# Performance work log

Hardware: AMD Instinct MI355X
Metric: run time of the kernel (lower is better)

Reference implementation:

```python
import jax, jax.numpy as jnp
import numpy as np

C = 16          # cardinality (hard-coded in GraphHead)
E = 1024        # node_encoding_size == representation_size (residual requires equality)
S = 1024        # spatial_head output size (hard-coded Linear(256,1024))
R = 1024        # representation_size
D = R // C      # sub_repr_size = 64
NS, NO = 64, 256
NUM_ITER = 2
EPS = 1e-5


def _w(key, shape, fan_in):
    return jax.random.normal(key, shape, dtype=jnp.float32) * np.float32((2.0 / fan_in) ** 0.5)


def setup_inputs() -> dict:
    key = jax.random.key(0)
    ks = jax.random.split(key, 16)
    inp = {
        'h': jax.random.normal(ks[0], (NS, E), dtype=jnp.float32),
        'o': jax.random.normal(ks[1], (NO, E), dtype=jnp.float32),
        'spatial': jax.random.normal(ks[2], (NS, NO, S), dtype=jnp.float32),
        # attention_head: MultiBranchFusion(2E, 1024, R, 16)
        'att_w1': _w(ks[3], (C, 2 * E, D), 2 * E), 'att_b1': jnp.zeros((C, D), jnp.float32),
        'att_w2': _w(ks[4], (C, S, D), S),         'att_b2': jnp.zeros((C, D), jnp.float32),
        'att_w3': _w(ks[5], (C, D, R), D),         'att_b3': jnp.zeros((C, R), jnp.float32),
        # sub_to_obj: MessageMBF(E, 1024, R, 'subject', 16)
        's2o_w1': _w(ks[6], (C, E, D), E),         's2o_b1': jnp.zeros((C, D), jnp.float32),
        's2o_w2': _w(ks[7], (C, S, D), S),         's2o_b2': jnp.zeros((C, D), jnp.float32),
        's2o_w3': _w(ks[8], (C, D, R), D),         's2o_b3': jnp.zeros((C, R), jnp.float32),
        # obj_to_sub: MessageMBF(E, 1024, R, 'object', 16)
        'o2s_w1': _w(ks[9], (C, E, D), E),         'o2s_b1': jnp.zeros((C, D), jnp.float32),
        'o2s_w2': _w(ks[10], (C, S, D), S),        'o2s_b2': jnp.zeros((C, D), jnp.float32),
        'o2s_w3': _w(ks[11], (C, D, R), D),        'o2s_b3': jnp.zeros((C, R), jnp.float32),
        # adjacency: Linear(R, 1)
        'adj_w': _w(ks[12], (R, 1), R), 'adj_b': jnp.zeros((1,), jnp.float32),
        # LayerNorms
        'ns_g': jnp.ones((E,), jnp.float32), 'ns_b': jnp.zeros((E,), jnp.float32),
        'no_g': jnp.ones((E,), jnp.float32), 'no_b': jnp.zeros((E,), jnp.float32),
    }
    return inp


def _layernorm(x, g, b):
    m = jnp.mean(x, axis=-1, keepdims=True)
    v = jnp.mean((x - m) ** 2, axis=-1, keepdims=True)
    return (x - m) * jax.lax.rsqrt(v + EPS) * g + b


def _mbf_pair(app, spa, w1, b1, w2, b2, w3, b3):
    # app [ns,no,A], spa [ns,no,S] -> [ns,no,R]; sum over C branches of fc3(relu(fc1*fc2))
    a = jnp.einsum('ija,cad->cijd', app, w1) + b1[:, None, None, :]
    s = jnp.einsum('ijs,csd->cijd', spa, w2) + b2[:, None, None, :]
    g = jax.nn.relu(a * s)
    return jnp.einsum('cijd,cdr->ijr', g, w3) + b3.sum(0)


def _msg_subject(h, spa, w1, b1, w2, b2, w3, b3):
    # MessageMBF subject: broadcast fc1(h) [ns,d] against fc2(spa) [ns,no,d]
    a = jnp.einsum('ia,cad->cid', h, w1) + b1[:, None, :]
    s = jnp.einsum('ijs,csd->cijd', spa, w2) + b2[:, None, None, :]
    g = jax.nn.relu(a[:, :, None, :] * s)
    return jnp.einsum('cijd,cdr->ijr', g, w3) + b3.sum(0)  # [ns,no,R]


def _msg_object(o, spa, w1, b1, w2, b2, w3, b3):
    # MessageMBF object: broadcast fc1(o) [no,d] against fc2(spa) [ns,no,d]
    a = jnp.einsum('ja,cad->cjd', o, w1) + b1[:, None, :]
    s = jnp.einsum('ijs,csd->cijd', spa, w2) + b2[:, None, None, :]
    g = jax.nn.relu(a[:, None, :, :] * s)
    return jnp.einsum('cijd,cdr->ijr', g, w3) + b3.sum(0)  # [ns,no,R]


def reference(h, o, spatial,
              att_w1, att_b1, att_w2, att_b2, att_w3, att_b3,
              s2o_w1, s2o_b1, s2o_w2, s2o_b2, s2o_w3, s2o_b3,
              o2s_w1, o2s_b1, o2s_w2, o2s_b2, o2s_w3, o2s_b3,
              adj_w, adj_b, ns_g, ns_b, no_g, no_b):
    ns, no = h.shape[0], o.shape[0]
    for _ in range(NUM_ITER):
        # edge weights via attention MBF on concatenated pair encodings
        pair_app = jnp.concatenate([
            jnp.broadcast_to(h[:, None, :], (ns, no, E)),
            jnp.broadcast_to(o[None, :, :], (ns, no, E)),
        ], axis=-1)
        w = jax.nn.relu(_mbf_pair(pair_app, spatial, att_w1, att_b1, att_w2, att_b2, att_w3, att_b3))
        adj = jnp.einsum('ijr,rk->ij', w, adj_w) + adj_b[0]  # [ns,no]
        # update subject nodes from object messages
        m_o2s = _msg_object(o, spatial, o2s_w1, o2s_b1, o2s_w2, o2s_b2, o2s_w3, o2s_b3)
        msg_h = jax.nn.relu(jnp.einsum('ij,ijr->ir', jax.nn.softmax(adj, axis=1), m_o2s))
        h = _layernorm(h + msg_h, ns_g, ns_b)
        # update object nodes from (updated) subject messages
        m_s2o = _msg_subject(h, spatial, s2o_w1, s2o_b1, s2o_w2, s2o_b2, s2o_w3, s2o_b3)
        msg_o = jax.nn.relu(jnp.einsum('ij,ijr->jr', jax.nn.softmax(adj, axis=0), m_s2o))
        o = _layernorm(o + msg_o, no_g, no_b)
    return jnp.concatenate([h, o], axis=0)  # [ns+no, E]
```

## Files before the change

kernel.cpp:

```cpp
#include <hip/hip_runtime.h>
#include <cstdint>
#include <cstddef>

typedef _Float16 hf;
typedef _Float16 h8v __attribute__((ext_vector_type(8)));
typedef float f4v __attribute__((ext_vector_type(4)));

#define NS 64
#define NO 256
#define MP 16384
#define KD 1024

__device__ __forceinline__ h8v cvt8(float4 a, float4 b) {
    h8v r;
    r[0] = (hf)a.x; r[1] = (hf)a.y; r[2] = (hf)a.z; r[3] = (hf)a.w;
    r[4] = (hf)b.x; r[5] = (hf)b.y; r[6] = (hf)b.z; r[7] = (hf)b.w;
    return r;
}
__device__ __forceinline__ float f4at(const float4& a, const float4& b, int e) {
    const float* p = e < 4 ? (const float*)&a : (const float*)&b;
    return p[e & 3];
}

__global__ void k_reorder16(const float* __restrict__ src, hf* __restrict__ dhi,
                            hf* __restrict__ dlo, int Asrc, int aOff) {
    __shared__ float tile[64][65];
    int c = blockIdx.x, a0 = blockIdx.y * 64;
    int t = threadIdx.x, lx = t & 63, ly = t >> 6;
#pragma unroll
    for (int p = 0; p < 16; ++p) {
        int ar = ly + p * 4;
        tile[ar][lx] = src[(size_t)(c * Asrc + aOff + a0 + ar) * 64 + lx];
    }
    __syncthreads();
#pragma unroll
    for (int p = 0; p < 16; ++p) {
        int d = ly + p * 4;
        float v = tile[lx][d];
        hf h = (hf)v;
        size_t idx = (size_t)(c * 64 + d) * 1024 + a0 + lx;
        dhi[idx] = h;
        if (dlo) dlo[idx] = (hf)(v - (float)h);
    }
}

__global__ void k_transpose16(const float* __restrict__ src, hf* __restrict__ dhi,
                              hf* __restrict__ dlo) {
    __shared__ float tile[64][65];
    int r0 = blockIdx.x * 64, s0 = blockIdx.y * 64;
    int t = threadIdx.x, lx = t & 63, ly = t >> 6;
#pragma unroll
    for (int p = 0; p < 16; ++p) {
        int srow = ly + p * 4;
        tile[srow][lx] = src[(size_t)(s0 + srow) * 1024 + r0 + lx];
    }
    __syncthreads();
#pragma unroll
    for (int p = 0; p < 16; ++p) {
        int rr = ly + p * 4;
        float v = tile[lx][rr];
        hf h = (hf)v;
        size_t idx = (size_t)(r0 + rr) * 1024 + s0 + lx;
        dhi[idx] = h;
        if (dlo) dlo[idx] = (hf)(v - (float)h);
    }
}

__global__ void k_prep_bc(const float* __restrict__ ab2, const float* __restrict__ ob2,
                          const float* __restrict__ sb2, const float* __restrict__ ab3,
                          const float* __restrict__ ob3, const float* __restrict__ sb3,
                          float* __restrict__ b2cat, float* __restrict__ b3a,
                          float* __restrict__ b3o, float* __restrict__ b3s) {
    int g = blockIdx.x * 256 + threadIdx.x;
    if (g >= 1024) return;
    b2cat[g] = ab2[g]; b2cat[1024 + g] = ob2[g]; b2cat[2048 + g] = sb2[g];
    float sa = 0.f, so = 0.f, ss = 0.f;
    for (int c = 0; c < 16; ++c) {
        sa += ab3[c * 1024 + g];
        so += ob3[c * 1024 + g];
        ss += sb3[c * 1024 + g];
    }
    b3a[g] = sa; b3o[g] = so; b3s[g] = ss;
}

__global__ void k_init_ho(const float* __restrict__ h, const float* __restrict__ o,
                          float* __restrict__ outbuf, hf* __restrict__ h16, hf* __restrict__ o16) {
    int g = blockIdx.x * 256 + threadIdx.x;
    if (g < NS * KD) { float v = h[g]; outbuf[g] = v; h16[g] = (hf)v; }
    int g2 = g - NS * KD;
    if (g2 >= 0 && g2 < NO * KD) { float v = o[g2]; outbuf[NS * KD + g2] = v; o16[g2] = (hf)v; }
}

__global__ __launch_bounds__(256) void k_prep_gemm(
    const float* __restrict__ sp,
    const hf* __restrict__ Wah, const hf* __restrict__ Wal,
    const hf* __restrict__ Wo2, const hf* __restrict__ Ws2,
    const float* __restrict__ b2cat,
    hf* __restrict__ Sh, hf* __restrict__ Sl,
    hf* __restrict__ So, hf* __restrict__ Ss) {
    __shared__ hf Ah[4096];
    __shared__ hf Bh[4096];
    __shared__ hf Bl[4096];
    const int tid = threadIdx.x;
    int lin = blockIdx.y * 24 + blockIdx.x;
    int xcd = lin & 7, slot = lin >> 3;
    int xn = slot % 24;
    const int plane = xn >> 3;
    const int nloc = (xn & 7) * 128;
    const int m0 = ((xcd << 4) + slot / 24) * 128;
    const hf* Bb = plane == 0 ? Wah : (plane == 1 ? Wo2 : Ws2);
    const bool hasL = (plane == 0);
    const int lane = tid & 63, wid = tid >> 6;
    const int wm = wid >> 1, wn = wid & 1;
    const int lr = lane & 15, lg = lane >> 4;
    const int srow = tid >> 2, sseg = tid & 3;
    const int wo_ = srow * 32 + (sseg ^ ((srow >> 1) & 3)) * 8;
    const int rsl = (lg ^ ((lr >> 1) & 3)) * 8;

    f4v acc[4][4];
    f4v zz; zz[0] = 0.f; zz[1] = 0.f; zz[2] = 0.f; zz[3] = 0.f;
#pragma unroll
    for (int a = 0; a < 4; ++a)
#pragma unroll
        for (int b = 0; b < 4; ++b) acc[a][b] = zz;

    const float* pa0 = sp + (size_t)(m0 + srow) * KD + sseg * 8;
    const float* pa1 = sp + (size_t)(m0 + 64 + srow) * KD + sseg * 8;
    const hf* pb0 = Bb + (size_t)(nloc + srow) * KD + sseg * 8;
    const hf* pb1 = Bb + (size_t)(nloc + 64 + srow) * KD + sseg * 8;
    const hf* ql0 = Wal + (size_t)(nloc + srow) * KD + sseg * 8;
    const hf* ql1 = Wal + (size_t)(nloc + 64 + srow) * KD + sseg * 8;

    float4 a00, a01, a10, a11;
    h8v vb0, vb1, wb0, wb1;
    auto LOAD = [&](int kk) {
        a00 = *(const float4*)(pa0 + kk); a01 = *(const float4*)(pa0 + kk + 4);
        a10 = *(const float4*)(pa1 + kk); a11 = *(const float4*)(pa1 + kk + 4);
        vb0 = *(const h8v*)(pb0 + kk); vb1 = *(const h8v*)(pb1 + kk);
        if (hasL) { wb0 = *(const h8v*)(ql0 + kk); wb1 = *(const h8v*)(ql1 + kk); }
    };
    LOAD(0);
    for (int t = 0; t < 32; ++t) {
        __syncthreads();
        *(h8v*)(Ah + wo_) = cvt8(a00, a01);
        *(h8v*)(Ah + 2048 + wo_) = cvt8(a10, a11);
        *(h8v*)(Bh + wo_) = vb0; *(h8v*)(Bh + 2048 + wo_) = vb1;
        if (hasL) { *(h8v*)(Bl + wo_) = wb0; *(h8v*)(Bl + 2048 + wo_) = wb1; }
        __syncthreads();
        if (t + 1 < 32) LOAD((t + 1) * 32);
        h8v fa[4], fb[4];
#pragma unroll
        for (int x = 0; x < 4; ++x) {
            fa[x] = *(const h8v*)(Ah + (wm * 64 + x * 16 + lr) * 32 + rsl);
            fb[x] = *(const h8v*)(Bh + (wn * 64 + x * 16 + lr) * 32 + rsl);
        }
#pragma unroll
        for (int mi = 0; mi < 4; ++mi)
#pragma unroll
            for (int ni = 0; ni < 4; ++ni)
                acc[mi][ni] = __builtin_amdgcn_mfma_f32_16x16x32_f16(fa[mi], fb[ni], acc[mi][ni], 0, 0, 0);
        if (hasL) {
#pragma unroll
            for (int x = 0; x < 4; ++x)
                fb[x] = *(const h8v*)(Bl + (wn * 64 + x * 16 + lr) * 32 + rsl);
#pragma unroll
            for (int mi = 0; mi < 4; ++mi)
#pragma unroll
                for (int ni = 0; ni < 4; ++ni)
                    acc[mi][ni] = __builtin_amdgcn_mfma_f32_16x16x32_f16(fa[mi], fb[ni], acc[mi][ni], 0, 0, 0);
        }
    }
#pragma unroll
    for (int mi = 0; mi < 4; ++mi)
#pragma unroll
        for (int ni = 0; ni < 4; ++ni)
#pragma unroll
            for (int r = 0; r < 4; ++r) {
                int gr = m0 + wm * 64 + mi * 16 + lg * 4 + r;
                int col = nloc + wn * 64 + ni * 16 + lr;
                float v = acc[mi][ni][r] + b2cat[plane * 1024 + col];
                size_t idx = (size_t)gr * KD + col;
                if (plane == 0) {
                    hf hi = (hf)v;
                    Sh[idx] = hi; Sl[idx] = (hf)(v - (float)hi);
                } else if (plane == 1) So[idx] = (hf)v;
                else Ss[idx] = (hf)v;
            }
}

__global__ void k_build_g(const hf* __restrict__ Sh, const hf* __restrict__ Sl,
                          const float* __restrict__ e1, const float* __restrict__ e2,
                          hf* __restrict__ Gh, hf* __restrict__ Gl) {
    int g = blockIdx.x * 256 + threadIdx.x;
    size_t base = (size_t)g * 8;
    int m = (int)(base >> 10);
    int k = (int)(base & 1023);
    int i = m >> 8, j = m & 255;
    h8v sh = *(const h8v*)(Sh + base);
    h8v sl = *(const h8v*)(Sl + base);
    float4 ex0 = *(const float4*)(e1 + (size_t)i * KD + k);
    float4 ex1 = *(const float4*)(e1 + (size_t)i * KD + k + 4);
    float4 ey0 = *(const float4*)(e2 + (size_t)j * KD + k);
    float4 ey1 = *(const float4*)(e2 + (size_t)j * KD + k + 4);
    h8v gh, gl;
#pragma unroll
    for (int e = 0; e < 8; ++e) {
        float s = (float)sh[e] + (float)sl[e];
        float ee = f4at(ex0, ex1, e) + f4at(ey0, ey1, e);
        float gg = ee * s; gg = gg > 0.f ? gg : 0.f;
        hf hi = (hf)gg; gh[e] = hi; gl[e] = (hf)(gg - (float)hi);
    }
    *(h8v*)(Gh + base) = gh;
    *(h8v*)(Gl + base) = gl;
}

__global__ __launch_bounds__(256) void k_adj_gemm(
    const hf* __restrict__ Gh, const hf* __restrict__ Gl,
    const hf* __restrict__ W3h, const hf* __restrict__ W3l,
    const float* __restrict__ b3, const float* __restrict__ aw,
    float* __restrict__ adjv) {
    __shared__ hf Ah[4096];
    __shared__ hf Al[4096];
    __shared__ hf Bh[4096];
    __shared__ hf Bl[4096];
    const int tid = threadIdx.x;
    int lin = blockIdx.y * 8 + blockIdx.x;
    int xcd = lin & 7, slot = lin >> 3;
    const int n0 = (slot & 7) * 128;
    const int m0 = ((xcd << 4) + (slot >> 3)) * 128;
    const int lane = tid & 63, wid = tid >> 6;
    const int wm = wid >> 1, wn = wid & 1;
    const int lr = lane & 15, lg = lane >> 4;
    const int srow = tid >> 2, sseg = tid & 3;
    const int wo_ = srow * 32 + (sseg ^ ((srow >> 1) & 3)) * 8;
    const int rsl = (lg ^ ((lr >> 1) & 3)) * 8;
    const int ar0 = m0 + srow, ar1 = ar0 + 64;
    const int ko = sseg * 8;

    f4v acc[4][4];
    f4v zz; zz[0] = 0.f; zz[1] = 0.f; zz[2] = 0.f; zz[3] = 0.f;
#pragma unroll
    for (int a = 0; a < 4; ++a)
#pragma unroll
        for (int b = 0; b < 4; ++b) acc[a][b] = zz;

    h8v va0, va1, ua0, ua1, vb0, vb1, wb0, wb1;
    auto LOAD = [&](int kk) {
        va0 = *(const h8v*)(Gh + (size_t)ar0 * KD + ko + kk);
        va1 = *(const h8v*)(Gh + (size_t)ar1 * KD + ko + kk);
        ua0 = *(const h8v*)(Gl + (size_t)ar0 * KD + ko + kk);
        ua1 = *(const h8v*)(Gl + (size_t)ar1 * KD + ko + kk);
        vb0 = *(const h8v*)(W3h + (size_t)(n0 + srow) * KD + ko + kk);
        vb1 = *(const h8v*)(W3h + (size_t)(n0 + 64 + srow) * KD + ko + kk);
        wb0 = *(const h8v*)(W3l + (size_t)(n0 + srow) * KD + ko + kk);
        wb1 = *(const h8v*)(W3l + (size_t)(n0 + 64 + srow) * KD + ko + kk);
    };
    LOAD(0);
    for (int t = 0; t < 32; ++t) {
        __syncthreads();
        *(h8v*)(Ah + wo_) = va0; *(h8v*)(Ah + 2048 + wo_) = va1;
        *(h8v*)(Al + wo_) = ua0; *(h8v*)(Al + 2048 + wo_) = ua1;
        *(h8v*)(Bh + wo_) = vb0; *(h8v*)(Bh + 2048 + wo_) = vb1;
        *(h8v*)(Bl + wo_) = wb0; *(h8v*)(Bl + 2048 + wo_) = wb1;
        __syncthreads();
        if (t + 1 < 32) LOAD((t + 1) * 32);
        h8v fa[4], fb[4];
#pragma unroll
        for (int x = 0; x < 4; ++x) {
            fa[x] = *(const h8v*)(Ah + (wm * 64 + x * 16 + lr) * 32 + rsl);
            fb[x] = *(const h8v*)(Bh + (wn * 64 + x * 16 + lr) * 32 + rsl);
        }
#pragma unroll
        for (int mi = 0; mi < 4; ++mi)
#pragma unroll
            for (int ni = 0; ni < 4; ++ni)
                acc[mi][ni] = __builtin_amdgcn_mfma_f32_16x16x32_f16(fa[mi], fb[ni], acc[mi][ni], 0, 0, 0);
#pragma unroll
        for (int x = 0; x < 4; ++x)
            fb[x] = *(const h8v*)(Bl + (wn * 64 + x * 16 + lr) * 32 + rsl);
#pragma unroll
        for (int mi = 0; mi < 4; ++mi)
#pragma unroll
            for (int ni = 0; ni < 4; ++ni)
                acc[mi][ni] = __builtin_amdgcn_mfma_f32_16x16x32_f16(fa[mi], fb[ni], acc[mi][ni], 0, 0, 0);
#pragma unroll
        for (int x = 0; x < 4; ++x) {
            fa[x] = *(const h8v*)(Al + (wm * 64 + x * 16 + lr) * 32 + rsl);
            fb[x] = *(const h8v*)(Bh + (wn * 64 + x * 16 + lr) * 32 + rsl);
        }
#pragma unroll
        for (int mi = 0; mi < 4; ++mi)
#pragma unroll
            for (int ni = 0; ni < 4; ++ni)
                acc[mi][ni] = __builtin_amdgcn_mfma_f32_16x16x32_f16(fa[mi], fb[ni], acc[mi][ni], 0, 0, 0);
    }
    float b3v[4], awv[4];
#pragma unroll
    for (int ni = 0; ni < 4; ++ni) {
        int gc = n0 + wn * 64 + ni * 16 + lr;
        b3v[ni] = b3[gc]; awv[ni] = aw[gc];
    }
#pragma unroll
    for (int mi = 0; mi < 4; ++mi)
#pragma unroll
        for (int r = 0; r < 4; ++r) {
            float part = 0.f;
#pragma unroll
            for (int ni = 0; ni < 4; ++ni) {
                float w = acc[mi][ni][r] + b3v[ni];
                w = w > 0.f ? w : 0.f;
                part += w * awv[ni];
            }
            part += __shfl_xor(part, 1);
            part += __shfl_xor(part, 2);
            part += __shfl_xor(part, 4);
            part += __shfl_xor(part, 8);
            if (lr == 0) atomicAdd(adjv + m0 + wm * 64 + mi * 16 + lg * 4 + r, part);
        }
}

struct SRoute { const hf* A; const hf* Bh; const hf* Bl; float* C; const float* bias; int m0; int M; };
struct SRoutes { SRoute r[5]; };

__global__ __launch_bounds__(256) void k_small(SRoutes RR) {
    const SRoute rt = RR.r[blockIdx.y];
    __shared__ hf Ah[4096];
    __shared__ hf Bh[4096];
    __shared__ hf Bl[4096];
    const int tid = threadIdx.x;
    const int n0 = blockIdx.x * 128;
    const int kbeg = blockIdx.z * 128;
    const int lane = tid & 63, wid = tid >> 6;
    const int wm = wid >> 1, wn = wid & 1;
    const int lr = lane & 15, lg = lane >> 4;
    const int srow = tid >> 2, sseg = tid & 3;
    const int wo_ = srow * 32 + (sseg ^ ((srow >> 1) & 3)) * 8;
    const int rsl = (lg ^ ((lr >> 1) & 3)) * 8;
    int ar0 = rt.m0 + srow;      if (ar0 >= rt.M) ar0 = rt.M - 1;
    int ar1 = rt.m0 + 64 + srow; if (ar1 >= rt.M) ar1 = rt.M - 1;
    const bool hasL = rt.Bl != nullptr;
    const int ko = kbeg + sseg * 8;

    f4v acc[4][4];
    f4v zz; zz[0] = 0.f; zz[1] = 0.f; zz[2] = 0.f; zz[3] = 0.f;
#pragma unroll
    for (int a = 0; a < 4; ++a)
#pragma unroll
        for (int b = 0; b < 4; ++b) acc[a][b] = zz;

    h8v va0, va1, vb0, vb1, wb0, wb1;
    auto LOAD = [&](int kk) {
        va0 = *(const h8v*)(rt.A + (size_t)ar0 * KD + ko + kk);
        va1 = *(const h8v*)(rt.A + (size_t)ar1 * KD + ko + kk);
        vb0 = *(const h8v*)(rt.Bh + (size_t)(n0 + srow) * KD + ko + kk);
        vb1 = *(const h8v*)(rt.Bh + (size_t)(n0 + 64 + srow) * KD + ko + kk);
        if (hasL) {
            wb0 = *(const h8v*)(rt.Bl + (size_t)(n0 + srow) * KD + ko + kk);
            wb1 = *(const h8v*)(rt.Bl + (size_t)(n0 + 64 + srow) * KD + ko + kk);
        }
    };
    LOAD(0);
    for (int t = 0; t < 4; ++t) {
        __syncthreads();
        *(h8v*)(Ah + wo_) = va0; *(h8v*)(Ah + 2048 + wo_) = va1;
        *(h8v*)(Bh + wo_) = vb0; *(h8v*)(Bh + 2048 + wo_) = vb1;
        if (hasL) { *(h8v*)(Bl + wo_) = wb0; *(h8v*)(Bl + 2048 + wo_) = wb1; }
        __syncthreads();
        if (t + 1 < 4) LOAD((t + 1) * 32);
        h8v fa[4], fb[4];
#pragma unroll
        for (int x = 0; x < 4; ++x) {
            fa[x] = *(const h8v*)(Ah + (wm * 64 + x * 16 + lr) * 32 + rsl);
            fb[x] = *(const h8v*)(Bh + (wn * 64 + x * 16 + lr) * 32 + rsl);
        }
#pragma unroll
        for (int mi = 0; mi < 4; ++mi)
#pragma unroll
            for (int ni = 0; ni < 4; ++ni)
                acc[mi][ni] = __builtin_amdgcn_mfma_f32_16x16x32_f16(fa[mi], fb[ni], acc[mi][ni], 0, 0, 0);
        if (hasL) {
#pragma unroll
            for (int x = 0; x < 4; ++x)
                fb[x] = *(const h8v*)(Bl + (wn * 64 + x * 16 + lr) * 32 + rsl);
#pragma unroll
            for (int mi = 0; mi < 4; ++mi)
#pragma unroll
                for (int ni = 0; ni < 4; ++ni)
                    acc[mi][ni] = __builtin_amdgcn_mfma_f32_16x16x32_f16(fa[mi], fb[ni], acc[mi][ni], 0, 0, 0);
        }
    }
#pragma unroll
    for (int mi = 0; mi < 4; ++mi)
#pragma unroll
        for (int ni = 0; ni < 4; ++ni)
#pragma unroll
            for (int r = 0; r < 4; ++r) {
                int gr = rt.m0 + wm * 64 + mi * 16 + lg * 4 + r;
                int gc = n0 + wn * 64 + ni * 16 + lr;
                if (gr < rt.M) {
                    float v = acc[mi][ni][r];
                    if (rt.bias && blockIdx.z == 0) v += rt.bias[gc];
                    atomicAdd(rt.C + (size_t)gr * KD + gc, v);
                }
            }
}

__global__ void k_softmax_rows(const float* __restrict__ adj, float* __restrict__ p) {
    __shared__ float red[256];
    int i = blockIdx.x, j = threadIdx.x;
    float x = adj[i * 256 + j];
    red[j] = x; __syncthreads();
    for (int s = 128; s > 0; s >>= 1) { if (j < s) red[j] = fmaxf(red[j], red[j + s]); __syncthreads(); }
    float mx = red[0]; __syncthreads();
    float e = __expf(x - mx);
    red[j] = e; __syncthreads();
    for (int s = 128; s > 0; s >>= 1) { if (j < s) red[j] += red[j + s]; __syncthreads(); }
    p[i * 256 + j] = e / red[0];
}

__global__ void k_softmax_cols(const float* __restrict__ adj, float* __restrict__ q) {
    int j = blockIdx.x, i = threadIdx.x;
    float x = adj[i * 256 + j];
    float mx = x;
#pragma unroll
    for (int off = 32; off > 0; off >>= 1) mx = fmaxf(mx, __shfl_xor(mx, off));
    float e = __expf(x - mx);
    float s = e;
#pragma unroll
    for (int off = 32; off > 0; off >>= 1) s += __shfl_xor(s, off);
    q[i * 256 + j] = e / s;
}

__global__ void k_build_Gh(const hf* __restrict__ S, const float* __restrict__ aF,
                           const float* __restrict__ p, hf* __restrict__ Gh) {
    __shared__ float pl[256];
    int i = blockIdx.x;
    int k = blockIdx.y * 256 + threadIdx.x;
    pl[threadIdx.x] = p[i * 256 + threadIdx.x];
    __syncthreads();
    const hf* sp = S + (size_t)(i * 256) * KD + k;
    float acc = 0.f;
#pragma unroll 4
    for (int j = 0; j < 256; ++j) {
        float a = aF[(size_t)j * KD + k];
        float s = (float)sp[(size_t)j * KD];
        float g = a * s; g = g > 0.f ? g : 0.f;
        acc += pl[j] * g;
    }
    Gh[(size_t)i * KD + k] = (hf)acc;
}

__global__ void k_build_Go(const hf* __restrict__ S, const float* __restrict__ aF,
                           const float* __restrict__ q, hf* __restrict__ Go) {
    __shared__ float ql[64];
    int j = blockIdx.x;
    int k = blockIdx.y * 256 + threadIdx.x;
    if (threadIdx.x < 64) ql[threadIdx.x] = q[threadIdx.x * 256 + j];
    __syncthreads();
    const hf* sp = S + (size_t)j * KD + k;
    float acc = 0.f;
#pragma unroll 4
    for (int i = 0; i < 64; ++i) {
        float a = aF[(size_t)i * KD + k];
        float s = (float)sp[(size_t)(i * 256) * KD];
        float g = a * s; g = g > 0.f ? g : 0.f;
        acc += ql[i] * g;
    }
    Go[(size_t)j * KD + k] = (hf)acc;
}

__global__ void k_ln_update(float* __restrict__ x, const float* __restrict__ msg,
                            const float* __restrict__ b3, const float* __restrict__ gamma,
                            const float* __restrict__ beta, hf* __restrict__ x16) {
    __shared__ float red[256];
    int r = blockIdx.x, t = threadIdx.x;
    float v[4];
    float s = 0.f;
#pragma unroll
    for (int e = 0; e < 4; ++e) {
        int idx = t + e * 256;
        float mm = msg[(size_t)r * KD + idx] + b3[idx];
        mm = mm > 0.f ? mm : 0.f;
        v[e] = x[(size_t)r * KD + idx] + mm;
        s += v[e];
    }
    red[t] = s; __syncthreads();
    for (int st = 128; st > 0; st >>= 1) { if (t < st) red[t] += red[t + st]; __syncthreads(); }
    float mean = red[0] * (1.f / 1024.f);
    __syncthreads();
    float s2 = 0.f;
#pragma unroll
    for (int e = 0; e < 4; ++e) { float d = v[e] - mean; s2 += d * d; }
    red[t] = s2; __syncthreads();
    for (int st = 128; st > 0; st >>= 1) { if (t < st) red[t] += red[t + st]; __syncthreads(); }
    float var = red[0] * (1.f / 1024.f);
    float rstd = rsqrtf(var + 1e-5f);
#pragma unroll
    for (int e = 0; e < 4; ++e) {
        int idx = t + e * 256;
        float y = (v[e] - mean) * rstd * gamma[idx] + beta[idx];
        x[(size_t)r * KD + idx] = y;
        x16[(size_t)r * KD + idx] = (hf)y;
    }
}

extern "C" void kernel_launch(void* const* d_in, const int* in_sizes, int n_in,
                              void* d_out, int out_size, void* d_ws, size_t ws_size,
                              hipStream_t stream) {
    const float* h_in    = (const float*)d_in[0];
    const float* o_in    = (const float*)d_in[1];
    const float* spatial = (const float*)d_in[2];
    const float* att_w1  = (const float*)d_in[3];
    const float* att_b1  = (const float*)d_in[4];
    const float* att_w2  = (const float*)d_in[5];
    const float* att_b2  = (const float*)d_in[6];
    const float* att_w3  = (const float*)d_in[7];
    const float* att_b3  = (const float*)d_in[8];
    const float* s2o_w1  = (const float*)d_in[9];
    const float* s2o_b1  = (const float*)d_in[10];
    const float* s2o_w2  = (const float*)d_in[11];
    const float* s2o_b2  = (const float*)d_in[12];
    const float* s2o_w3  = (const float*)d_in[13];
    const float* s2o_b3  = (const float*)d_in[14];
    const float* o2s_w1  = (const float*)d_in[15];
    const float* o2s_b1  = (const float*)d_in[16];
    const float* o2s_w2  = (const float*)d_in[17];
    const float* o2s_b2  = (const float*)d_in[18];
    const float* o2s_w3  = (const float*)d_in[19];
    const float* o2s_b3  = (const float*)d_in[20];
    const float* adj_w   = (const float*)d_in[21];
    const float* ns_g    = (const float*)d_in[23];
    const float* ns_b    = (const float*)d_in[24];
    const float* no_g    = (const float*)d_in[25];
    const float* no_b    = (const float*)d_in[26];

    char* ws = (char*)d_ws;
    size_t off = 0;
    auto alloc = [&](size_t bytes) -> char* {
        char* pp = ws + off;
        off += (bytes + 255) & ~(size_t)255;
        return pp;
    };
    const size_t PLANE = (size_t)MP * KD * sizeof(hf);
    const size_t WMAT  = (size_t)1024 * 1024 * sizeof(hf);
    hf* S_att_h = (hf*)alloc(PLANE);
    hf* S_att_l = (hf*)alloc(PLANE);
    hf* S_o2s   = (hf*)alloc(PLANE);
    hf* S_s2o   = (hf*)alloc(PLANE);
    hf* gA_h    = (hf*)alloc(PLANE);
    hf* gA_l    = (hf*)alloc(PLANE);
    hf* W2att_h = (hf*)alloc(WMAT); hf* W2att_l = (hf*)alloc(WMAT);
    hf* W2o2s   = (hf*)alloc(WMAT);
    hf* W2s2o   = (hf*)alloc(WMAT);
    hf* W1ah_h  = (hf*)alloc(WMAT); hf* W1ah_l  = (hf*)alloc(WMAT);
    hf* W1ao_h  = (hf*)alloc(WMAT); hf* W1ao_l  = (hf*)alloc(WMAT);
    hf* W1o2s   = (hf*)alloc(WMAT);
    hf* W1s2o   = (hf*)alloc(WMAT);
    hf* W3a_h   = (hf*)alloc(WMAT); hf* W3a_l   = (hf*)alloc(WMAT);
    hf* W3o     = (hf*)alloc(WMAT);
    hf* W3s     = (hf*)alloc(WMAT);
    float* b2cat = (float*)alloc(3072 * 4);
    float* b3a   = (float*)alloc(1024 * 4);
    float* b3o   = (float*)alloc(1024 * 4);
    float* b3s   = (float*)alloc(1024 * 4);
    float* fc1h = (float*)alloc((size_t)NS * KD * 4);
    float* fc1o = (float*)alloc((size_t)NO * KD * 4);
    float* aO2S = (float*)alloc((size_t)NO * KD * 4);
    float* aS2O = (float*)alloc((size_t)NS * KD * 4);
    float* msgh = (float*)alloc((size_t)NS * KD * 4);
    float* msgo = (float*)alloc((size_t)NO * KD * 4);
    float* adjv = (float*)alloc((size_t)MP * 4);
    char* zend_ = (char*)(adjv + MP);
    size_t zlen = (size_t)(zend_ - (char*)fc1h);
    float* pbuf = (float*)alloc((size_t)MP * 4);
    float* qbuf = (float*)alloc((size_t)MP * 4);
    hf* h16 = (hf*)alloc((size_t)NS * KD * sizeof(hf));
    hf* o16 = (hf*)alloc((size_t)NO * KD * sizeof(hf));
    hf* Gh  = (hf*)alloc((size_t)NS * KD * sizeof(hf));
    hf* Go  = (hf*)alloc((size_t)NO * KD * sizeof(hf));

    float* hbuf = (float*)d_out;
    float* obuf = (float*)d_out + NS * KD;

    k_reorder16<<<dim3(16, 16), 256, 0, stream>>>(att_w2, W2att_h, W2att_l, 1024, 0);
    k_reorder16<<<dim3(16, 16), 256, 0, stream>>>(o2s_w2, W2o2s, nullptr, 1024, 0);
    k_reorder16<<<dim3(16, 16), 256, 0, stream>>>(s2o_w2, W2s2o, nullptr, 1024, 0);
    k_reorder16<<<dim3(16, 16), 256, 0, stream>>>(att_w1, W1ah_h, W1ah_l, 2048, 0);
    k_reorder16<<<dim3(16, 16), 256, 0, stream>>>(att_w1, W1ao_h, W1ao_l, 2048, 1024);
    k_reorder16<<<dim3(16, 16), 256, 0, stream>>>(o2s_w1, W1o2s, nullptr, 1024, 0);
    k_reorder16<<<dim3(16, 16), 256, 0, stream>>>(s2o_w1, W1s2o, nullptr, 1024, 0);
    k_transpose16<<<dim3(16, 16), 256, 0, stream>>>(att_w3, W3a_h, W3a_l);
    k_transpose16<<<dim3(16, 16), 256, 0, stream>>>(o2s_w3, W3o, nullptr);
    k_transpose16<<<dim3(16, 16), 256, 0, stream>>>(s2o_w3, W3s, nullptr);
    k_prep_bc<<<dim3(4), 256, 0, stream>>>(att_b2, o2s_b2, s2o_b2, att_b3, o2s_b3, s2o_b3,
                                           b2cat, b3a, b3o, b3s);
    k_init_ho<<<dim3(1280), 256, 0, stream>>>(h_in, o_in, (float*)d_out, h16, o16);
    k_prep_gemm<<<dim3(24, 128), 256, 0, stream>>>(spatial, W2att_h, W2att_l, W2o2s, W2s2o,
                                                   b2cat, S_att_h, S_att_l, S_o2s, S_s2o);

    for (int it = 0; it < 2; ++it) {
        hipMemsetAsync(fc1h, 0, zlen, stream);
        {
            SRoutes R;
            R.r[0] = { h16, W1ah_h, W1ah_l, fc1h, att_b1, 0,   NS };
            R.r[1] = { o16, W1ao_h, W1ao_l, fc1o, nullptr, 0,   NO };
            R.r[2] = { o16, W1ao_h, W1ao_l, fc1o, nullptr, 128, NO };
            R.r[3] = { o16, W1o2s,  nullptr, aO2S, o2s_b1, 0,   NO };
            R.r[4] = { o16, W1o2s,  nullptr, aO2S, o2s_b1, 128, NO };
            k_small<<<dim3(8, 5, 8), 256, 0, stream>>>(R);
        }
        k_build_g<<<dim3(MP * KD / 8 / 256), 256, 0, stream>>>(S_att_h, S_att_l, fc1h, fc1o, gA_h, gA_l);
        k_adj_gemm<<<dim3(8, 128), 256, 0, stream>>>(gA_h, gA_l, W3a_h, W3a_l, b3a, adj_w, adjv);
        k_softmax_rows<<<dim3(NS), 256, 0, stream>>>(adjv, pbuf);
        k_softmax_cols<<<dim3(NO), 64, 0, stream>>>(adjv, qbuf);
        k_build_Gh<<<dim3(NS, 4), 256, 0, stream>>>(S_o2s, aO2S, pbuf, Gh);
        {
            SRoutes R;
            R.r[0] = { Gh, W3o, nullptr, msgh, nullptr, 0, NS };
            k_small<<<dim3(8, 1, 8), 256, 0, stream>>>(R);
        }
        k_ln_update<<<dim3(NS), 256, 0, stream>>>(hbuf, msgh, b3o, ns_g, ns_b, h16);
        {
            SRoutes R;
            R.r[0] = { h16, W1s2o, nullptr, aS2O, s2o_b1, 0, NS };
            k_small<<<dim3(8, 1, 8), 256, 0, stream>>>(R);
        }
        k_build_Go<<<dim3(NO, 4), 256, 0, stream>>>(S_s2o, aS2O, qbuf, Go);
        {
            SRoutes R;
            R.r[0] = { Go, W3s, nullptr, msgo, nullptr, 0,   NO };
            R.r[1] = { Go, W3s, nullptr, msgo, nullptr, 128, NO };
            k_small<<<dim3(8, 2, 8), 256, 0, stream>>>(R);
        }
        k_ln_update<<<dim3(NO), 256, 0, stream>>>(obuf, msgo, b3s, no_g, no_b, o16);
    }
    (void)in_sizes; (void)n_in; (void)out_size; (void)ws_size;
}
```

Measured before the change: 746.8 us.

## Widen GEMM N-tiles to 256, pre-pack spatial to fp16, batch weight reorder launches

Both k_prep_gemm and k_adj_gemm now compute a 128x256 output tile per block instead of 128x128. Each A tile is reused across twice as many columns, which halves redundant A loads; the cost is doubled accumulator registers and a launch_bounds occupancy hint of 2. The fp32 spatial tensor is converted once to fp16 in a separate pack kernel, reusing the gA_h buffer, so the prep GEMM reads half-width A data. The separate weight reorder and transpose launches are merged into two batched launches using blockIdx.z.

```diff
diff --git a/kernel.cpp b/kernel.cpp
--- a/kernel.cpp
+++ b/kernel.cpp
@@ -22,15 +22,25 @@
     return p[e & 3];
 }
 
-__global__ void k_reorder16(const float* __restrict__ src, hf* __restrict__ dhi,
-                            hf* __restrict__ dlo, int Asrc, int aOff) {
+__global__ void k_pack16(const float* __restrict__ src, hf* __restrict__ dst, int n8) {
+    int g = blockIdx.x * 256 + threadIdx.x;
+    if (g >= n8) return;
+    const float4* s4 = (const float4*)src;
+    float4 a = s4[2 * g], b = s4[2 * g + 1];
+    *(h8v*)(dst + (size_t)g * 8) = cvt8(a, b);
+}
+
+struct RoR { const float* src; hf* dhi; hf* dlo; int Asrc; int aOff; };
+struct RoRs { RoR r[7]; };
+__global__ void k_reorder16b(RoRs RR) {
+    const RoR rt = RR.r[blockIdx.z];
     __shared__ float tile[64][65];
     int c = blockIdx.x, a0 = blockIdx.y * 64;
     int t = threadIdx.x, lx = t & 63, ly = t >> 6;
 #pragma unroll
     for (int p = 0; p < 16; ++p) {
         int ar = ly + p * 4;
-        tile[ar][lx] = src[(size_t)(c * Asrc + aOff + a0 + ar) * 64 + lx];
+        tile[ar][lx] = rt.src[(size_t)(c * rt.Asrc + rt.aOff + a0 + ar) * 64 + lx];
     }
     __syncthreads();
 #pragma unroll
@@ -39,20 +49,22 @@
         float v = tile[lx][d];
         hf h = (hf)v;
         size_t idx = (size_t)(c * 64 + d) * 1024 + a0 + lx;
-        dhi[idx] = h;
-        if (dlo) dlo[idx] = (hf)(v - (float)h);
-    }
-}
-
-__global__ void k_transpose16(const float* __restrict__ src, hf* __restrict__ dhi,
-                              hf* __restrict__ dlo) {
+        rt.dhi[idx] = h;
+        if (rt.dlo) rt.dlo[idx] = (hf)(v - (float)h);
+    }
+}
+
+struct TrR { const float* src; hf* dhi; hf* dlo; };
+struct TrRs { TrR r[3]; };
+__global__ void k_transpose16b(TrRs RR) {
+    const TrR rt = RR.r[blockIdx.z];
     __shared__ float tile[64][65];
     int r0 = blockIdx.x * 64, s0 = blockIdx.y * 64;
     int t = threadIdx.x, lx = t & 63, ly = t >> 6;
 #pragma unroll
     for (int p = 0; p < 16; ++p) {
         int srow = ly + p * 4;
-        tile[srow][lx] = src[(size_t)(s0 + srow) * 1024 + r0 + lx];
+        tile[srow][lx] = rt.src[(size_t)(s0 + srow) * 1024 + r0 + lx];
     }
     __syncthreads();
 #pragma unroll
@@ -61,8 +73,8 @@
         float v = tile[lx][rr];
         hf h = (hf)v;
         size_t idx = (size_t)(r0 + rr) * 1024 + s0 + lx;
-        dhi[idx] = h;
-        if (dlo) dlo[idx] = (hf)(v - (float)h);
+        rt.dhi[idx] = h;
+        if (rt.dlo) rt.dlo[idx] = (hf)(v - (float)h);
     }
 }
 
@@ -91,23 +103,23 @@
     if (g2 >= 0 && g2 < NO * KD) { float v = o[g2]; outbuf[NS * KD + g2] = v; o16[g2] = (hf)v; }
 }
 
-__global__ __launch_bounds__(256) void k_prep_gemm(
-    const float* __restrict__ sp,
+__global__ __launch_bounds__(256, 2) void k_prep_gemm(
+    const hf* __restrict__ sp16,
     const hf* __restrict__ Wah, const hf* __restrict__ Wal,
     const hf* __restrict__ Wo2, const hf* __restrict__ Ws2,
     const float* __restrict__ b2cat,
     hf* __restrict__ Sh, hf* __restrict__ Sl,
     hf* __restrict__ So, hf* __restrict__ Ss) {
     __shared__ hf Ah[4096];
-    __shared__ hf Bh[4096];
-    __shared__ hf Bl[4096];
+    __shared__ hf Bh[8192];
+    __shared__ hf Bl[8192];
     const int tid = threadIdx.x;
-    int lin = blockIdx.y * 24 + blockIdx.x;
+    int lin = blockIdx.y * 12 + blockIdx.x;
     int xcd = lin & 7, slot = lin >> 3;
-    int xn = slot % 24;
-    const int plane = xn >> 3;
-    const int nloc = (xn & 7) * 128;
-    const int m0 = ((xcd << 4) + slot / 24) * 128;
+    int xn = slot % 12;
+    const int m0 = ((xcd << 4) + slot / 12) * 128;
+    const int plane = xn >> 2;
+    const int nbase = (xn & 3) * 256;
     const hf* Bb = plane == 0 ? Wah : (plane == 1 ? Wo2 : Ws2);
     const bool hasL = (plane == 0);
     const int lane = tid & 63, wid = tid >> 6;
@@ -117,75 +129,93 @@
     const int wo_ = srow * 32 + (sseg ^ ((srow >> 1) & 3)) * 8;
     const int rsl = (lg ^ ((lr >> 1) & 3)) * 8;
 
-    f4v acc[4][4];
+    f4v acc[2][4][4];
     f4v zz; zz[0] = 0.f; zz[1] = 0.f; zz[2] = 0.f; zz[3] = 0.f;
 #pragma unroll
-    for (int a = 0; a < 4; ++a)
-#pragma unroll
-        for (int b = 0; b < 4; ++b) acc[a][b] = zz;
-
-    const float* pa0 = sp + (size_t)(m0 + srow) * KD + sseg * 8;
-    const float* pa1 = sp + (size_t)(m0 + 64 + srow) * KD + sseg * 8;
-    const hf* pb0 = Bb + (size_t)(nloc + srow) * KD + sseg * 8;
-    const hf* pb1 = Bb + (size_t)(nloc + 64 + srow) * KD + sseg * 8;
-    const hf* ql0 = Wal + (size_t)(nloc + srow) * KD + sseg * 8;
-    const hf* ql1 = Wal + (size_t)(nloc + 64 + srow) * KD + sseg * 8;
-
-    float4 a00, a01, a10, a11;
-    h8v vb0, vb1, wb0, wb1;
+    for (int u = 0; u < 2; ++u)
+#pragma unroll
+        for (int a = 0; a < 4; ++a)
+#pragma unroll
+            for (int b = 0; b < 4; ++b) acc[u][a][b] = zz;
+
+    const int ko = sseg * 8;
+    const hf* pa0 = sp16 + (size_t)(m0 + srow) * KD + ko;
+    const hf* pa1 = sp16 + (size_t)(m0 + 64 + srow) * KD + ko;
+    const hf* pb00 = Bb + (size_t)(nbase + srow) * KD + ko;
+    const hf* pb01 = Bb + (size_t)(nbase + 64 + srow) * KD + ko;
+    const hf* pb10 = Bb + (size_t)(nbase + 128 + srow) * KD + ko;
+    const hf* pb11 = Bb + (size_t)(nbase + 192 + srow) * KD + ko;
+    const hf* ql00 = Wal + (size_t)(nbase + srow) * KD + ko;
+    const hf* ql01 = Wal + (size_t)(nbase + 64 + srow) * KD + ko;
+    const hf* ql10 = Wal + (size_t)(nbase + 128 + srow) * KD + ko;
+    const hf* ql11 = Wal + (size_t)(nbase + 192 + srow) * KD + ko;
+
+    h8v va0, va1, vb00, vb01, vb10, vb11, wb00, wb01, wb10, wb11;
     auto LOAD = [&](int kk) {
-        a00 = *(const float4*)(pa0 + kk); a01 = *(const float4*)(pa0 + kk + 4);
-        a10 = *(const float4*)(pa1 + kk); a11 = *(const float4*)(pa1 + kk + 4);
-        vb0 = *(const h8v*)(pb0 + kk); vb1 = *(const h8v*)(pb1 + kk);
-        if (hasL) { wb0 = *(const h8v*)(ql0 + kk); wb1 = *(const h8v*)(ql1 + kk); }
+        va0 = *(const h8v*)(pa0 + kk); va1 = *(const h8v*)(pa1 + kk);
+        vb00 = *(const h8v*)(pb00 + kk); vb01 = *(const h8v*)(pb01 + kk);
+        vb10 = *(const h8v*)(pb10 + kk); vb11 = *(const h8v*)(pb11 + kk);
+        if (hasL) {
+            wb00 = *(const h8v*)(ql00 + kk); wb01 = *(const h8v*)(ql01 + kk);
+            wb10 = *(const h8v*)(ql10 + kk); wb11 = *(const h8v*)(ql11 + kk);
+        }
     };
     LOAD(0);
     for (int t = 0; t < 32; ++t) {
         __syncthreads();
-        *(h8v*)(Ah + wo_) = cvt8(a00, a01);
-        *(h8v*)(Ah + 2048 + wo_) = cvt8(a10, a11);
-        *(h8v*)(Bh + wo_) = vb0; *(h8v*)(Bh + 2048 + wo_) = vb1;
-        if (hasL) { *(h8v*)(Bl + wo_) = wb0; *(h8v*)(Bl + 2048 + wo_) = wb1; }
+        *(h8v*)(Ah + wo_) = va0; *(h8v*)(Ah + 2048 + wo_) = va1;
+        *(h8v*)(Bh + wo_) = vb00; *(h8v*)(Bh + 2048 + wo_) = vb01;
+        *(h8v*)(Bh + 4096 + wo_) = vb10; *(h8v*)(Bh + 6144 + wo_) = vb11;
+        if (hasL) {
+            *(h8v*)(Bl + wo_) = wb00; *(h8v*)(Bl + 2048 + wo_) = wb01;
+            *(h8v*)(Bl + 4096 + wo_) = wb10; *(h8v*)(Bl + 6144 + wo_) = wb11;
+        }
         __syncthreads();
         if (t + 1 < 32) LOAD((t + 1) * 32);
         h8v fa[4], fb[4];
 #pragma unroll
-        for (int x = 0; x < 4; ++x) {
+        for (int x = 0; x < 4; ++x)
             fa[x] = *(const h8v*)(Ah + (wm * 64 + x * 16 + lr) * 32 + rsl);
-            fb[x] = *(const h8v*)(Bh + (wn * 64 + x * 16 + lr) * 32 + rsl);
-        }
+#pragma unroll
+        for (int u = 0; u < 2; ++u) {
+#pragma unroll
+            for (int x = 0; x < 4; ++x)
+                fb[x] = *(const h8v*)(Bh + u * 4096 + (wn * 64 + x * 16 + lr) * 32 + rsl);
+#pragma unroll
+            for (int mi = 0; mi < 4; ++mi)
+#pragma unroll
+                for (int ni = 0; ni < 4; ++ni)
+                    acc[u][mi][ni] = __builtin_amdgcn_mfma_f32_16x16x32_f16(fa[mi], fb[ni], acc[u][mi][ni], 0, 0, 0);
+            if (hasL) {
+#pragma unroll
+                for (int x = 0; x < 4; ++x)
+                    fb[x] = *(const h8v*)(Bl + u * 4096 + (wn * 64 + x * 16 + lr) * 32 + rsl);
+#pragma unroll
+                for (int mi = 0; mi < 4; ++mi)
+#pragma unroll
+                    for (int ni = 0; ni < 4; ++ni)
+                        acc[u][mi][ni] = __builtin_amdgcn_mfma_f32_16x16x32_f16(fa[mi], fb[ni], acc[u][mi][ni], 0, 0, 0);
+            }
+        }
+    }
+#pragma unroll
+    for (int u = 0; u < 2; ++u)
 #pragma unroll
         for (int mi = 0; mi < 4; ++mi)
 #pragma unroll
             for (int ni = 0; ni < 4; ++ni)
-                acc[mi][ni] = __builtin_amdgcn_mfma_f32_16x16x32_f16(fa[mi], fb[ni], acc[mi][ni], 0, 0, 0);
-        if (hasL) {
-#pragma unroll
-            for (int x = 0; x < 4; ++x)
-                fb[x] = *(const h8v*)(Bl + (wn * 64 + x * 16 + lr) * 32 + rsl);
-#pragma unroll
-            for (int mi = 0; mi < 4; ++mi)
-#pragma unroll
-                for (int ni = 0; ni < 4; ++ni)
-                    acc[mi][ni] = __builtin_amdgcn_mfma_f32_16x16x32_f16(fa[mi], fb[ni], acc[mi][ni], 0, 0, 0);
-        }
-    }
-#pragma unroll
-    for (int mi = 0; mi < 4; ++mi)
-#pragma unroll
-        for (int ni = 0; ni < 4; ++ni)
-#pragma unroll
-            for (int r = 0; r < 4; ++r) {
-                int gr = m0 + wm * 64 + mi * 16 + lg * 4 + r;
-                int col = nloc + wn * 64 + ni * 16 + lr;
-                float v = acc[mi][ni][r] + b2cat[plane * 1024 + col];
-                size_t idx = (size_t)gr * KD + col;
-                if (plane == 0) {
-                    hf hi = (hf)v;
-                    Sh[idx] = hi; Sl[idx] = (hf)(v - (float)hi);
-                } else if (plane == 1) So[idx] = (hf)v;
-                else Ss[idx] = (hf)v;
-            }
+#pragma unroll
+                for (int r = 0; r < 4; ++r) {
+                    int gr = m0 + wm * 64 + mi * 16 + lg * 4 + r;
+                    int col = nbase + u * 128 + wn * 64 + ni * 16 + lr;
+                    float v = acc[u][mi][ni][r] + b2cat[plane * 1024 + col];
+                    size_t idx = (size_t)gr * KD + col;
+                    if (plane == 0) {
+                        hf hi = (hf)v;
+                        Sh[idx] = hi; Sl[idx] = (hf)(v - (float)hi);
+                    } else if (plane == 1) So[idx] = (hf)v;
+                    else Ss[idx] = (hf)v;
+                }
 }
 
 __global__ void k_build_g(const hf* __restrict__ Sh, const hf* __restrict__ Sl,
@@ -214,20 +244,20 @@
     *(h8v*)(Gl + base) = gl;
 }
 
-__global__ __launch_bounds__(256) void k_adj_gemm(
+__global__ __launch_bounds__(256, 2) void k_adj_gemm(
     const hf* __restrict__ Gh, const hf* __restrict__ Gl,
     const hf* __restrict__ W3h, const hf* __restrict__ W3l,
     const float* __restrict__ b3, const float* __restrict__ aw,
     float* __restrict__ adjv) {
     __shared__ hf Ah[4096];
     __shared__ hf Al[4096];
-    __shared__ hf Bh[4096];
-    __shared__ hf Bl[4096];
+    __shared__ hf Bh[8192];
+    __shared__ hf Bl[8192];
     const int tid = threadIdx.x;
-    int lin = blockIdx.y * 8 + blockIdx.x;
+    int lin = blockIdx.y * 4 + blockIdx.x;
     int xcd = lin & 7, slot = lin >> 3;
-    const int n0 = (slot & 7) * 128;
-    const int m0 = ((xcd << 4) + (slot >> 3)) * 128;
+    const int nbase = (slot & 3) * 256;
+    const int m0 = ((xcd << 4) + (slot >> 2)) * 128;
     const int lane = tid & 63, wid = tid >> 6;
     const int wm = wid >> 1, wn = wid & 1;
     const int lr = lane & 15, lg = lane >> 4;
@@ -237,80 +267,94 @@
     const int ar0 = m0 + srow, ar1 = ar0 + 64;
     const int ko = sseg * 8;
 
-    f4v acc[4][4];
+    f4v acc[2][4][4];
     f4v zz; zz[0] = 0.f; zz[1] = 0.f; zz[2] = 0.f; zz[3] = 0.f;
 #pragma unroll
-    for (int a = 0; a < 4; ++a)
-#pragma unroll
-        for (int b = 0; b < 4; ++b) acc[a][b] = zz;
-
-    h8v va0, va1, ua0, ua1, vb0, vb1, wb0, wb1;
+    for (int u = 0; u < 2; ++u)
+#pragma unroll
+        for (int a = 0; a < 4; ++a)
+#pragma unroll
+            for (int b = 0; b < 4; ++b) acc[u][a][b] = zz;
+
+    h8v va0, va1, ua0, ua1;
+    h8v vb00, vb01, vb10, vb11, wb00, wb01, wb10, wb11;
     auto LOAD = [&](int kk) {
         va0 = *(const h8v*)(Gh + (size_t)ar0 * KD + ko + kk);
         va1 = *(const h8v*)(Gh + (size_t)ar1 * KD + ko + kk);
         ua0 = *(const h8v*)(Gl + (size_t)ar0 * KD + ko + kk);
         ua1 = *(const h8v*)(Gl + (size_t)ar1 * KD + ko + kk);
-        vb0 = *(const h8v*)(W3h + (size_t)(n0 + srow) * KD + ko + kk);
-        vb1 = *(const h8v*)(W3h + (size_t)(n0 + 64 + srow) * KD + ko + kk);
-        wb0 = *(const h8v*)(W3l + (size_t)(n0 + srow) * KD + ko + kk);
-        wb1 = *(const h8v*)(W3l + (size_t)(n0 + 64 + srow) * KD + ko + kk);
+        vb00 = *(const h8v*)(W3h + (size_t)(nbase + srow) * KD + ko + kk);
+        vb01 = *(const h8v*)(W3h + (size_t)(nbase + 64 + srow) * KD + ko + kk);
+        vb10 = *(const h8v*)(W3h + (size_t)(nbase + 128 + srow) * KD + ko + kk);
+        vb11 = *(const h8v*)(W3h + (size_t)(nbase + 192 + srow) * KD + ko + kk);
+        wb00 = *(const h8v*)(W3l + (size_t)(nbase + srow) * KD + ko + kk);
+        wb01 = *(const h8v*)(W3l + (size_t)(nbase + 64 + srow) * KD + ko + kk);
+        wb10 = *(const h8v*)(W3l + (size_t)(nbase + 128 + srow) * KD + ko + kk);
+        wb11 = *(const h8v*)(W3l + (size_t)(nbase + 192 + srow) * KD + ko + kk);
     };
     LOAD(0);
     for (int t = 0; t < 32; ++t) {
         __syncthreads();
         *(h8v*)(Ah + wo_) = va0; *(h8v*)(Ah + 2048 + wo_) = va1;
         *(h8v*)(Al + wo_) = ua0; *(h8v*)(Al + 2048 + wo_) = ua1;
-        *(h8v*)(Bh + wo_) = vb0; *(h8v*)(Bh + 2048 + wo_) = vb1;
-        *(h8v*)(Bl + wo_) = wb0; *(h8v*)(Bl + 2048 + wo_) = wb1;
+        *(h8v*)(Bh + wo_) = vb00; *(h8v*)(Bh + 2048 + wo_) = vb01;
+        *(h8v*)(Bh + 4096 + wo_) = vb10; *(h8v*)(Bh + 6144 + wo_) = vb11;
+        *(h8v*)(Bl + wo_) = wb00; *(h8v*)(Bl + 2048 + wo_) = wb01;
+        *(h8v*)(Bl + 4096 + wo_) = wb10; *(h8v*)(Bl + 6144 + wo_) = wb11;
         __syncthreads();
         if (t + 1 < 32) LOAD((t + 1) * 32);
-        h8v fa[4], fb[4];
+        h8v fa[4], fal[4], fb[4];
 #pragma unroll
         for (int x = 0; x < 4; ++x) {
-            fa[x] = *(const h8v*)(Ah + (wm * 64 + x * 16 + lr) * 32 + rsl);
-            fb[x] = *(const h8v*)(Bh + (wn * 64 + x * 16 + lr) * 32 + rsl);
-        }
-#pragma unroll
-        for (int mi = 0; mi < 4; ++mi)
-#pragma unroll
-            for (int ni = 0; ni < 4; ++ni)
-                acc[mi][ni] = __builtin_amdgcn_mfma_f32_16x16x32_f16(fa[mi], fb[ni], acc[mi][ni], 0, 0, 0);
-#pragma unroll
-        for (int x = 0; x < 4; ++x)
-            fb[x] = *(const h8v*)(Bl + (wn * 64 + x * 16 + lr) * 32 + rsl);
-#pragma unroll
-        for (int mi = 0; mi < 4; ++mi)
-#pragma unroll
-            for (int ni = 0; ni < 4; ++ni)
-                acc[mi][ni] = __builtin_amdgcn_mfma_f32_16x16x32_f16(fa[mi], fb[ni], acc[mi][ni], 0, 0, 0);
-#pragma unroll
-        for (int x = 0; x < 4; ++x) {
-            fa[x] = *(const h8v*)(Al + (wm * 64 + x * 16 + lr) * 32 + rsl);
-            fb[x] = *(const h8v*)(Bh + (wn * 64 + x * 16 + lr) * 32 + rsl);
-        }
-#pragma unroll
-        for (int mi = 0; mi < 4; ++mi)
-#pragma unroll
-            for (int ni = 0; ni < 4; ++ni)
-                acc[mi][ni] = __builtin_amdgcn_mfma_f32_16x16x32_f16(fa[mi], fb[ni], acc[mi][ni], 0, 0, 0);
-    }
-    float b3v[4], awv[4];
-#pragma unroll
-    for (int ni = 0; ni < 4; ++ni) {
-        int gc = n0 + wn * 64 + ni * 16 + lr;
-        b3v[ni] = b3[gc]; awv[ni] = aw[gc];
-    }
+            fa[x]  = *(const h8v*)(Ah + (wm * 64 + x * 16 + lr) * 32 + rsl);
+            fal[x] = *(const h8v*)(Al + (wm * 64 + x * 16 + lr) * 32 + rsl);
+        }
+#pragma unroll
+        for (int u = 0; u < 2; ++u) {
+#pragma unroll
+            for (int x = 0; x < 4; ++x)
+                fb[x] = *(const h8v*)(Bh + u * 4096 + (wn * 64 + x * 16 + lr) * 32 + rsl);
+#pragma unroll
+            for (int mi = 0; mi < 4; ++mi)
+#pragma unroll
+                for (int ni = 0; ni < 4; ++ni)
+                    acc[u][mi][ni] = __builtin_amdgcn_mfma_f32_16x16x32_f16(fa[mi], fb[ni], acc[u][mi][ni], 0, 0, 0);
+#pragma unroll
+            for (int mi = 0; mi < 4; ++mi)
+#pragma unroll
+                for (int ni = 0; ni < 4; ++ni)
+                    acc[u][mi][ni] = __builtin_amdgcn_mfma_f32_16x16x32_f16(fal[mi], fb[ni], acc[u][mi][ni], 0, 0, 0);
+#pragma unroll
+            for (int x = 0; x < 4; ++x)
+                fb[x] = *(const h8v*)(Bl + u * 4096 + (wn * 64 + x * 16 + lr) * 32 + rsl);
+#pragma unroll
+            for (int mi = 0; mi < 4; ++mi)
+#pragma unroll
+                for (int ni = 0; ni < 4; ++ni)
+                    acc[u][mi][ni] = __builtin_amdgcn_mfma_f32_16x16x32_f16(fa[mi], fb[ni], acc[u][mi][ni], 0, 0, 0);
+        }
+    }
+    float b3v[2][4], awv[2][4];
+#pragma unroll
+    for (int u = 0; u < 2; ++u)
+#pragma unroll
+        for (int ni = 0; ni < 4; ++ni) {
+            int gc = nbase + u * 128 + wn * 64 + ni * 16 + lr;
+            b3v[u][ni] = b3[gc]; awv[u][ni] = aw[gc];
+        }
 #pragma unroll
     for (int mi = 0; mi < 4; ++mi)
 #pragma unroll
         for (int r = 0; r < 4; ++r) {
             float part = 0.f;
 #pragma unroll
-            for (int ni = 0; ni < 4; ++ni) {
-                float w = acc[mi][ni][r] + b3v[ni];
-                w = w > 0.f ? w : 0.f;
-                part += w * awv[ni];
-            }
+            for (int u = 0; u < 2; ++u)
+#pragma unroll
+                for (int ni = 0; ni < 4; ++ni) {
+                    float w = acc[u][mi][ni][r] + b3v[u][ni];
+                    w = w > 0.f ? w : 0.f;
+                    part += w * awv[u][ni];
+                }
             part += __shfl_xor(part, 1);
             part += __shfl_xor(part, 2);
             part += __shfl_xor(part, 4);
@@ -549,6 +593,7 @@
     hf* S_s2o   = (hf*)alloc(PLANE);
     hf* gA_h    = (hf*)alloc(PLANE);
     hf* gA_l    = (hf*)alloc(PLANE);
+    hf* sp16    = gA_h;
     hf* W2att_h = (hf*)alloc(WMAT); hf* W2att_l = (hf*)alloc(WMAT);
     hf* W2o2s   = (hf*)alloc(WMAT);
     hf* W2s2o   = (hf*)alloc(WMAT);
@@ -582,20 +627,29 @@
     float* hbuf = (float*)d_out;
     float* obuf = (float*)d_out + NS * KD;
 
-    k_reorder16<<<dim3(16, 16), 256, 0, stream>>>(att_w2, W2att_h, W2att_l, 1024, 0);
-    k_reorder16<<<dim3(16, 16), 256, 0, stream>>>(o2s_w2, W2o2s, nullptr, 1024, 0);
-    k_reorder16<<<dim3(16, 16), 256, 0, stream>>>(s2o_w2, W2s2o, nullptr, 1024, 0);
-    k_reorder16<<<dim3(16, 16), 256, 0, stream>>>(att_w1, W1ah_h, W1ah_l, 2048, 0);
-    k_reorder16<<<dim3(16, 16), 256, 0, stream>>>(att_w1, W1ao_h, W1ao_l, 2048, 1024);
-    k_reorder16<<<dim3(16, 16), 256, 0, stream>>>(o2s_w1, W1o2s, nullptr, 1024, 0);
-    k_reorder16<<<dim3(16, 16), 256, 0, stream>>>(s2o_w1, W1s2o, nullptr, 1024, 0);
-    k_transpose16<<<dim3(16, 16), 256, 0, stream>>>(att_w3, W3a_h, W3a_l);
-    k_transpose16<<<dim3(16, 16), 256, 0, stream>>>(o2s_w3, W3o, nullptr);
-    k_transpose16<<<dim3(16, 16), 256, 0, stream>>>(s2o_w3, W3s, nullptr);
+    k_pack16<<<dim3(MP * KD / 8 / 256), 256, 0, stream>>>(spatial, sp16, MP * KD / 8);
+    {
+        RoRs R;
+        R.r[0] = { att_w2, W2att_h, W2att_l, 1024, 0 };
+        R.r[1] = { o2s_w2, W2o2s, nullptr, 1024, 0 };
+        R.r[2] = { s2o_w2, W2s2o, nullptr, 1024, 0 };
+        R.r[3] = { att_w1, W1ah_h, W1ah_l, 2048, 0 };
+        R.r[4] = { att_w1, W1ao_h, W1ao_l, 2048, 1024 };
+        R.r[5] = { o2s_w1, W1o2s, nullptr, 1024, 0 };
+        R.r[6] = { s2o_w1, W1s2o, nullptr, 1024, 0 };
+        k_reorder16b<<<dim3(16, 16, 7), 256, 0, stream>>>(R);
+    }
+    {
+        TrRs T;
+        T.r[0] = { att_w3, W3a_h, W3a_l };
+        T.r[1] = { o2s_w3, W3o, nullptr };
+        T.r[2] = { s2o_w3, W3s, nullptr };
+        k_transpose16b<<<dim3(16, 16, 3), 256, 0, stream>>>(T);
+    }
     k_prep_bc<<<dim3(4), 256, 0, stream>>>(att_b2, o2s_b2, s2o_b2, att_b3, o2s_b3, s2o_b3,
                                            b2cat, b3a, b3o, b3s);
     k_init_ho<<<dim3(1280), 256, 0, stream>>>(h_in, o_in, (float*)d_out, h16, o16);
-    k_prep_gemm<<<dim3(24, 128), 256, 0, stream>>>(spatial, W2att_h, W2att_l, W2o2s, W2s2o,
+    k_prep_gemm<<<dim3(12, 128), 256, 0, stream>>>(sp16, W2att_h, W2att_l, W2o2s, W2s2o,
                                                    b2cat, S_att_h, S_att_l, S_o2s, S_s2o);
 
     for (int it = 0; it < 2; ++it) {
@@ -610,7 +664,7 @@
             k_small<<<dim3(8, 5, 8), 256, 0, stream>>>(R);
         }
         k_build_g<<<dim3(MP * KD / 8 / 256), 256, 0, stream>>>(S_att_h, S_att_l, fc1h, fc1o, gA_h, gA_l);
-        k_adj_gemm<<<dim3(8, 128), 256, 0, stream>>>(gA_h, gA_l, W3a_h, W3a_l, b3a, adj_w, adjv);
+        k_adj_gemm<<<dim3(4, 128), 256, 0, stream>>>(gA_h, gA_l, W3a_h, W3a_l, b3a, adj_w, adjv);
         k_softmax_rows<<<dim3(NS), 256, 0, stream>>>(adjv, pbuf);
         k_softmax_cols<<<dim3(NO), 64, 0, stream>>>(adjv, qbuf);
         k_build_Gh<<<dim3(NS, 4), 256, 0, stream>>>(S_o2s, aO2S, pbuf, Gh);
```

New measurement: 682.3 us. -8.6%, faster.
